# Performance work log

Measured on AMD Instinct MI355X. Metric: run time of the kernel, lower is better.

## Reference

```python
import jax, jax.numpy as jnp
import numpy as np

H = 4
C = 140
N0, E0 = 20000, 320000
N1, E1 = 5000, 80000
N2, E2 = 20000 // 16, 20000
N2, E2 = 1250, 20000
NSAME = 10  # conv02,11,12,21,22,14,15,16,04,05 (all 140->140)


def _seg_mean(v, idx, n):
    s = jax.ops.segment_sum(v, idx, num_segments=n)
    cnt = jax.ops.segment_sum(jnp.ones((idx.shape[0],), v.dtype), idx, num_segments=n)
    return s / jnp.maximum(cnt, 1.0)[:, None]


def _feast_conv(x, ei, W, u, c, b, n):
    # PyG FeaStConv, mean aggregation, no self loops.
    src, dst = ei[0], ei[1]
    xj = x[src]               # (E, Cin) neighbor (source) features
    xi = x[dst]               # (E, Cin) center (target) features
    q = jax.nn.softmax((xj - xi) @ u + c, axis=-1)            # (E, H)
    m = (xj @ W).reshape(xj.shape[0], H, -1)                  # (E, H, Cout)
    msg = jnp.einsum('eh,ehc->ec', q, m)                      # (E, Cout)
    return _seg_mean(msg, dst, n) + b


def _ln(h, g, be):
    mu = h.mean(-1, keepdims=True)
    v = ((h - mu) ** 2).mean(-1, keepdims=True)
    return (h - mu) * jax.lax.rsqrt(v + 1e-5) * g + be


def _block(x, ei, n, W, u, c, b, g=None, be=None, sW=None, sb=None, relu=True):
    h = _feast_conv(x, ei, W, u, c, b, n)
    if g is not None:
        h = _ln(h, g, be)
    skip = x if sW is None else x @ sW + sb
    h = h + skip
    if relu:
        h = jax.nn.relu(h)
    return h


def setup_inputs() -> dict:
    key = jax.random.key(0)
    ks = iter(jax.random.split(key, 80))

    def nrm(shape, s=0.05):
        return jax.random.normal(next(ks), shape, jnp.float32) * s

    inp = {}
    inp['x'] = jax.random.normal(next(ks), (N0, 4), jnp.float32)
    inp['e0'] = jax.random.randint(next(ks), (2, E0), 0, N0)
    inp['e1'] = jax.random.randint(next(ks), (2, E1), 0, N1)
    inp['e2'] = jax.random.randint(next(ks), (2, E2), 0, N2)
    inp['cl1'] = jax.random.randint(next(ks), (N0,), 0, N1)
    inp['cl2'] = jax.random.randint(next(ks), (N1,), 0, N2)
    inp['n0'], inp['n1'], inp['n2'] = N0, N1, N2
    # conv01: 4 -> 140 (linear skip)
    inp['W01'] = nrm((4, H * C)); inp['u01'] = nrm((4, H)); inp['c01'] = nrm((H,))
    inp['b01'] = nrm((C,)); inp['sW01'] = nrm((4, C)); inp['sb01'] = nrm((C,))
    inp['g01'] = jnp.ones((C,)); inp['be01'] = jnp.zeros((C,))
    # 10 stacked 140->140 blocks (identity skip)
    inp['Ws'] = nrm((NSAME, C, H * C)); inp['us'] = nrm((NSAME, C, H))
    inp['cs'] = nrm((NSAME, H)); inp['bs'] = nrm((NSAME, C))
    inp['gs'] = jnp.ones((NSAME, C)); inp['bes'] = jnp.zeros((NSAME, C))
    # 2 concat blocks: 280 -> 140 (conv13, conv03), linear skip
    inp['Wc'] = nrm((2, 2 * C, H * C)); inp['uc'] = nrm((2, 2 * C, H))
    inp['cc'] = nrm((2, H)); inp['bc'] = nrm((2, C))
    inp['sWc'] = nrm((2, 2 * C, C)); inp['sbc'] = nrm((2, C))
    inp['gc'] = jnp.ones((2, C)); inp['bec'] = jnp.zeros((2, C))
    # conv06: 140 -> 1, no LN, no relu, linear skip
    inp['Wo'] = nrm((C, H * 1)); inp['uo'] = nrm((C, H)); inp['co'] = nrm((H,))
    inp['bo'] = nrm((1,)); inp['sWo'] = nrm((C, 1)); inp['sbo'] = nrm((1,))
    return inp


def reference(x, W01, u01, c01, b01, sW01, sb01, g01, be01,
              Ws, us, cs, bs, gs, bes,
              Wc, uc, cc, bc, sWc, sbc, gc, bec,
              Wo, uo, co, bo, sWo, sbo,
              e0, e1, e2, cl1, cl2, n0, n1, n2):
    def same(h, i, ei, n):
        return _block(h, ei, n, Ws[i], us[i], cs[i], bs[i], gs[i], bes[i])

    def catblk(h, i, ei, n):
        return _block(h, ei, n, Wc[i], uc[i], cc[i], bc[i], gc[i], bec[i], sWc[i], sbc[i])

    h = _block(x, e0, n0, W01, u01, c01, b01, g01, be01, sW01, sb01)  # conv01
    h = same(h, 0, e0, n0)                                            # conv02
    copy0 = h
    h1 = _seg_mean(h, cl1, n1)                                        # pool1
    h1 = same(h1, 1, e1, n1)                                          # conv11
    h1 = same(h1, 2, e1, n1)                                          # conv12
    copy1 = h1
    h2 = _seg_mean(h1, cl2, n2)                                       # pool2
    h2 = same(h2, 3, e2, n2)                                          # conv21
    h2 = same(h2, 4, e2, n2)                                          # conv22
    h1 = h2[cl2]                                                      # unpool2
    h1 = jnp.concatenate((h1, copy1), axis=1)
    h1 = catblk(h1, 0, e1, n1)                                        # conv13
    h1 = same(h1, 5, e1, n1)                                          # conv14
    h1 = same(h1, 6, e1, n1)                                          # conv15
    h1 = same(h1, 7, e1, n1)                                          # conv16
    h = h1[cl1]                                                       # unpool1
    h = jnp.concatenate((h, copy0), axis=1)
    h = catblk(h, 1, e0, n0)                                          # conv03
    h = same(h, 8, e0, n0)                                            # conv04
    h = same(h, 9, e0, n0)                                            # conv05
    h = _block(h, e0, n0, Wo, uo, co, bo, None, None, sWo, sbo, relu=False)  # conv06
    return h.reshape(-1, 1)
```

## Files before the change

### kernel.cpp

```cpp
#include <hip/hip_runtime.h>
#include <math.h>

#define HH 4
#define CC 140
#define HALF 160

typedef __attribute__((ext_vector_type(8))) short short8;
typedef __attribute__((ext_vector_type(8))) _Float16 half8;
typedef __attribute__((ext_vector_type(4))) float f32x4;
typedef __attribute__((ext_vector_type(2))) _Float16 h2;
typedef unsigned short u16;

__device__ inline u16 f2h(float x) {
  union { _Float16 h; u16 u; } v; v.h = (_Float16)x; return v.u;
}
__device__ inline float h2f(u16 u) {
  union { _Float16 h; u16 u; } v; v.u = u; return (float)v.h;
}
__device__ inline h2 u2h2(unsigned u) {
  union { unsigned u; h2 h; } v; v.u = u; return v.h;
}
__device__ inline float dot2(h2 a, h2 b, float c) {
#if __has_builtin(__builtin_amdgcn_fdot2)
  return __builtin_amdgcn_fdot2(a, b, c, false);
#else
  return c + (float)a[0] * (float)b[0] + (float)a[1] * (float)b[1];
#endif
}

__global__ __launch_bounds__(256) void k_zero_i32(int* __restrict__ p, int n) {
  int i = blockIdx.x * 256 + threadIdx.x;
  if (i < n) p[i] = 0;
}
__global__ __launch_bounds__(256) void k_hist_all(
    const int* __restrict__ e0, int nE0, const int* __restrict__ e1, int nE1,
    const int* __restrict__ e2, int nE2, const int* __restrict__ cl1, int n0,
    const int* __restrict__ cl2, int n1,
    int* __restrict__ c0, int* __restrict__ c1, int* __restrict__ c2,
    int* __restrict__ c3, int* __restrict__ c4) {
  int j = blockIdx.x * 256 + threadIdx.x;
  if (j < nE0) { atomicAdd(&c0[e0[nE0 + j]], 1); return; }
  j -= nE0;
  if (j < nE1) { atomicAdd(&c1[e1[nE1 + j]], 1); return; }
  j -= nE1;
  if (j < nE2) { atomicAdd(&c2[e2[nE2 + j]], 1); return; }
  j -= nE2;
  if (j < n0) { atomicAdd(&c3[cl1[j]], 1); return; }
  j -= n0;
  if (j < n1) { atomicAdd(&c4[cl2[j]], 1); }
}
__global__ __launch_bounds__(1024) void k_exscan5(
    int* __restrict__ c0, int n0, int* __restrict__ r0,
    int* __restrict__ c1, int n1, int* __restrict__ r1,
    int* __restrict__ c2, int n2, int* __restrict__ r2,
    int* __restrict__ c3, int n3, int* __restrict__ r3,
    int* __restrict__ c4, int n4, int* __restrict__ r4) {
  int* in; int n; int* out;
  switch (blockIdx.x) {
    case 0: in = c0; n = n0; out = r0; break;
    case 1: in = c1; n = n1; out = r1; break;
    case 2: in = c2; n = n2; out = r2; break;
    case 3: in = c3; n = n3; out = r3; break;
    default: in = c4; n = n4; out = r4; break;
  }
  __shared__ int buf[1024];
  __shared__ int carry_s;
  if (threadIdx.x == 0) carry_s = 0;
  __syncthreads();
  for (int base = 0; base < n; base += 1024) {
    int i = base + (int)threadIdx.x;
    int v = (i < n) ? in[i] : 0;
    buf[threadIdx.x] = v;
    __syncthreads();
    int x = v;
    for (int off = 1; off < 1024; off <<= 1) {
      int t = (threadIdx.x >= (unsigned)off) ? buf[threadIdx.x - off] : 0;
      __syncthreads();
      x += t;
      buf[threadIdx.x] = x;
      __syncthreads();
    }
    int carry = carry_s;
    if (i < n) {
      int pref = carry + x - v;
      out[i] = pref;
      in[i] = pref;
    }
    __syncthreads();
    if (threadIdx.x == 1023) carry_s = carry + buf[1023];
    __syncthreads();
  }
  if (threadIdx.x == 0) out[n] = carry_s;
}
__global__ __launch_bounds__(256) void k_scatter_all(
    const int* __restrict__ e0, int nE0, const int* __restrict__ e1, int nE1,
    const int* __restrict__ e2, int nE2, const int* __restrict__ cl1, int n0,
    const int* __restrict__ cl2, int n1,
    int* __restrict__ c0, int* __restrict__ c1, int* __restrict__ c2,
    int* __restrict__ c3, int* __restrict__ c4,
    int* __restrict__ s0, int* __restrict__ s1, int* __restrict__ s2,
    int* __restrict__ s3, int* __restrict__ s4) {
  int j = blockIdx.x * 256 + threadIdx.x;
  if (j < nE0) { int p = atomicAdd(&c0[e0[nE0 + j]], 1); s0[p] = e0[j]; return; }
  j -= nE0;
  if (j < nE1) { int p = atomicAdd(&c1[e1[nE1 + j]], 1); s1[p] = e1[j]; return; }
  j -= nE1;
  if (j < nE2) { int p = atomicAdd(&c2[e2[nE2 + j]], 1); s2[p] = e2[j]; return; }
  j -= nE2;
  if (j < n0) { int p = atomicAdd(&c3[cl1[j]], 1); s3[p] = j; return; }
  j -= n0;
  if (j < n1) { int p = atomicAdd(&c4[cl2[j]], 1); s4[p] = j; }
}

__device__ inline void pack_one(int idx, const float* __restrict__ W,
                                const float* __restrict__ u, const float* __restrict__ sW,
                                u16* __restrict__ out, int C, int K1, int K2, int Kpad) {
  int col = idx / Kpad, kp = idx - col * Kpad;
  int ksrc = -1;
  if (kp < K1) ksrc = kp;
  else if (kp >= HALF && kp - HALF < K2) ksrc = K1 + (kp - HALF);
  float v = 0.f;
  if (ksrc >= 0) {
    if (col < 4 * C) {
      int c = col >> 2, h = col & 3;
      v = W[(size_t)ksrc * 4 * C + h * C + c];
    } else if (col < 4 * C + 4) {
      v = u[(size_t)ksrc * 4 + (col - 4 * C)];
    } else if (sW && col < 5 * C + 4) {
      v = sW[(size_t)ksrc * C + (col - 4 * C - 4)];
    }
  }
  out[idx] = f2h(v);
}
#define P01 (704 * 32)
#define PCAT (704 * 320)
#define PO (64 * 160)
#define PS (576 * 160)
__global__ __launch_bounds__(256) void k_pack_all(
    const float* __restrict__ W01, const float* __restrict__ u01, const float* __restrict__ sW01,
    const float* __restrict__ Wc, const float* __restrict__ uc, const float* __restrict__ sWc,
    const float* __restrict__ Wo, const float* __restrict__ uo, const float* __restrict__ sWo,
    const float* __restrict__ Ws, const float* __restrict__ us,
    const float* __restrict__ x,
    u16* __restrict__ Bp01, u16* __restrict__ Bpc0, u16* __restrict__ Bpc1,
    u16* __restrict__ Bpo, u16* __restrict__ Bps_all, u16* __restrict__ xb, int N0) {
  int j = blockIdx.x * 256 + threadIdx.x;
  if (j < P01) { pack_one(j, W01, u01, sW01, Bp01, CC, 4, 0, 32); return; }
  j -= P01;
  if (j < PCAT) { pack_one(j, Wc, uc, sWc, Bpc0, CC, CC, CC, 320); return; }
  j -= PCAT;
  if (j < PCAT) {
    pack_one(j, Wc + (size_t)2 * CC * HH * CC, uc + (size_t)2 * CC * HH,
             sWc + (size_t)2 * CC * CC, Bpc1, CC, CC, CC, 320);
    return;
  }
  j -= PCAT;
  if (j < PO) { pack_one(j, Wo, uo, sWo, Bpo, 1, CC, 0, 160); return; }
  j -= PO;
  if (j < 10 * PS) {
    int layer = j / PS, r = j - layer * PS;
    pack_one(r, Ws + (size_t)layer * CC * 4 * CC, us + (size_t)layer * CC * 4, nullptr,
             Bps_all + (size_t)layer * PS, CC, CC, 0, 160);
    return;
  }
  j -= 10 * PS;
  if (j < N0 * 32) {
    int i = j >> 5, c = j & 31;
    xb[j] = f2h(c < 4 ? x[(size_t)i * 4 + c] : 0.f);
  }
}

__global__ __launch_bounds__(256) void k_gemm_mfma(
    const u16* __restrict__ A1, const u16* __restrict__ A2,
    const int* __restrict__ amap, const u16* __restrict__ Bp,
    u16* __restrict__ Gy, float* __restrict__ Gl, float* __restrict__ Gs,
    int yEnd, int Cs, int N, int Kpad, int lda1) {
  __shared__ __align__(16) u16 As[128 * 32];
  __shared__ __align__(16) u16 Bs[64 * 32];
  const int tid = threadIdx.x;
  const int row0 = blockIdx.y * 128, col0 = blockIdx.x * 64;
  const int w = tid >> 6, lane = tid & 63;
  const int wm = w >> 1, wn = w & 1;
  const int arow = lane & 15, chunk = lane >> 4;
  const int swz = chunk ^ (arow & 3);
  f32x4 acc[4][2];
#pragma unroll
  for (int i = 0; i < 4; ++i)
#pragma unroll
    for (int j = 0; j < 2; ++j) acc[i][j] = (f32x4){0.f, 0.f, 0.f, 0.f};
  const int sar = tid >> 1;
  const int sak = (tid & 1) * 16;
  const int sbc = tid >> 2;
  const int sbk = (tid & 3) * 8;
  for (int k0 = 0; k0 < Kpad; k0 += 32) {
    {
      int gr = row0 + sar;
      short8 v0 = {0, 0, 0, 0, 0, 0, 0, 0}, v1 = v0;
      if (gr < N) {
        int kp0 = k0 + sak;
        const u16* b_;
        int rr, kk, ld;
        if (A2 && kp0 >= HALF) {
          b_ = A2; rr = gr; kk = kp0 - HALF; ld = HALF;
        } else {
          b_ = A1; rr = amap ? amap[gr] : gr; kk = kp0; ld = lda1;
        }
        const u16* p = b_ + (size_t)rr * ld + kk;
        v0 = *(const short8*)(p);
        v1 = *(const short8*)(p + 8);
      }
      int c0 = sak >> 3, sw = sar & 3;
      *(short8*)(As + sar * 32 + ((c0 ^ sw) << 3)) = v0;
      *(short8*)(As + sar * 32 + (((c0 + 1) ^ sw) << 3)) = v1;
    }
    {
      int gc = col0 + sbc;
      short8 v = *(const short8*)(Bp + (size_t)gc * Kpad + k0 + sbk);
      int c = sbk >> 3, sw = sbc & 3;
      *(short8*)(Bs + sbc * 32 + ((c ^ sw) << 3)) = v;
    }
    __syncthreads();
    half8 bf[2], af[4];
#pragma unroll
    for (int ni = 0; ni < 2; ++ni) {
      int col = wn * 32 + ni * 16 + arow;
      bf[ni] = *(const half8*)(Bs + col * 32 + (swz << 3));
    }
#pragma unroll
    for (int mi = 0; mi < 4; ++mi) {
      int r = wm * 64 + mi * 16 + arow;
      af[mi] = *(const half8*)(As + r * 32 + (swz << 3));
    }
#pragma unroll
    for (int mi = 0; mi < 4; ++mi)
#pragma unroll
      for (int ni = 0; ni < 2; ++ni)
        acc[mi][ni] = __builtin_amdgcn_mfma_f32_16x16x32_f16(af[mi], bf[ni], acc[mi][ni], 0, 0, 0);
    __syncthreads();
  }
  const int crow = (lane >> 4) * 4, ccol = lane & 15;
#pragma unroll
  for (int mi = 0; mi < 4; ++mi) {
    int gr0 = row0 + wm * 64 + mi * 16 + crow;
#pragma unroll
    for (int ni = 0; ni < 2; ++ni) {
      int gc = col0 + wn * 32 + ni * 16 + ccol;
#pragma unroll
      for (int j = 0; j < 4; ++j) {
        int gr = gr0 + j;
        if (gr >= N) continue;
        float v = acc[mi][ni][j];
        if (gc < yEnd) Gy[(size_t)gr * yEnd + gc] = f2h(v);
        else if (gc < yEnd + 4) Gl[(size_t)gr * 4 + (gc - yEnd)] = v;
        else if (gc < yEnd + 4 + Cs) Gs[(size_t)gr * Cs + (gc - yEnd - 4)] = v;
      }
    }
  }
}

__global__ __launch_bounds__(256) void k_agg(
    const u16* __restrict__ Gy, const float* __restrict__ Gl,
    const float* __restrict__ cv, const float* __restrict__ bias,
    const float* __restrict__ g, const float* __restrict__ be,
    const u16* __restrict__ skipA,
    const float* __restrict__ Gs, const float* __restrict__ sb,
    const int* __restrict__ rp, const int* __restrict__ sl,
    u16* __restrict__ outA, int n, int relu) {
  int wid = blockIdx.x * 4 + ((int)threadIdx.x >> 6);
  int lane = threadIdx.x & 63;
  if (wid >= n) return;
  float4 la = *(const float4*)(Gl + (size_t)wid * 4);
  float d0 = cv[0] - la.x, d1 = cv[1] - la.y;
  float d2 = cv[2] - la.z, d3 = cv[3] - la.w;
  int eb = rp[wid], ee = rp[wid + 1];
  const int c0 = lane, c1 = lane + 64, c2 = lane + 128;
  const bool h2v = c2 < CC;
  float acc0 = 0.f, acc1 = 0.f, acc2 = 0.f;
  for (int base = eb; base < ee; base += 64) {
    int m = min(ee - base, 64);
    int sreg = 0;
    int q01 = 0, q23 = 0;
    if (lane < m) {
      sreg = sl[base + lane];
      float4 lg = *(const float4*)(Gl + (size_t)sreg * 4);
      float t0 = lg.x + d0, t1 = lg.y + d1, t2 = lg.z + d2, t3 = lg.w + d3;
      float mx = fmaxf(fmaxf(t0, t1), fmaxf(t2, t3));
      float q0 = __expf(t0 - mx), q1 = __expf(t1 - mx);
      float q2 = __expf(t2 - mx), q3 = __expf(t3 - mx);
      float qi = 1.f / (q0 + q1 + q2 + q3);
      q01 = (int)((unsigned)f2h(q0 * qi) | ((unsigned)f2h(q1 * qi) << 16));
      q23 = (int)((unsigned)f2h(q2 * qi) | ((unsigned)f2h(q3 * qi) << 16));
    }
#pragma unroll 2
    for (int j = 0; j < m; ++j) {
      int s = __shfl(sreg, j);
      h2 p01 = u2h2((unsigned)__shfl(q01, j));
      h2 p23 = u2h2((unsigned)__shfl(q23, j));
      const u16* gy = Gy + (size_t)s * 560;
      uint2 y0 = *(const uint2*)(gy + (c0 << 2));
      acc0 = dot2(u2h2(y0.x), p01, acc0);
      acc0 = dot2(u2h2(y0.y), p23, acc0);
      uint2 y1 = *(const uint2*)(gy + (c1 << 2));
      acc1 = dot2(u2h2(y1.x), p01, acc1);
      acc1 = dot2(u2h2(y1.y), p23, acc1);
      if (h2v) {
        uint2 y2 = *(const uint2*)(gy + (c2 << 2));
        acc2 = dot2(u2h2(y2.x), p01, acc2);
        acc2 = dot2(u2h2(y2.y), p23, acc2);
      }
    }
  }
  int cnt = ee - eb;
  float inv = 1.f / (float)(cnt > 1 ? cnt : 1);
  float v0 = acc0 * inv + bias[c0];
  float v1 = acc1 * inv + bias[c1];
  float v2 = h2v ? acc2 * inv + bias[c2] : 0.f;
  if (g) {
    float s1 = v0 + v1 + v2;
    float s2 = v0 * v0 + v1 * v1 + v2 * v2;
#pragma unroll
    for (int off = 32; off > 0; off >>= 1) {
      s1 += __shfl_xor(s1, off);
      s2 += __shfl_xor(s2, off);
    }
    float mu = s1 * (1.0f / CC);
    float var = s2 * (1.0f / CC) - mu * mu;
    float r = rsqrtf(var + 1e-5f);
    v0 = (v0 - mu) * r * g[c0] + be[c0];
    v1 = (v1 - mu) * r * g[c1] + be[c1];
    if (h2v) v2 = (v2 - mu) * r * g[c2] + be[c2];
  }
  if (skipA) {
    const u16* sk = skipA + (size_t)wid * HALF;
    v0 += h2f(sk[c0]);
    v1 += h2f(sk[c1]);
    if (h2v) v2 += h2f(sk[c2]);
  } else {
    const float* gsr = Gs + (size_t)wid * CC;
    v0 += gsr[c0] + sb[c0];
    v1 += gsr[c1] + sb[c1];
    if (h2v) v2 += gsr[c2] + sb[c2];
  }
  if (relu) {
    v0 = fmaxf(v0, 0.f); v1 = fmaxf(v1, 0.f); v2 = fmaxf(v2, 0.f);
  }
  u16* oa = outA + (size_t)wid * HALF;
  oa[c0] = f2h(v0);
  oa[c1] = f2h(v1);
  if (h2v) oa[c2] = f2h(v2);
  else if (c2 < HALF) oa[c2] = 0;
}

__global__ __launch_bounds__(256) void k_out(
    const u16* __restrict__ Gy, const float* __restrict__ Gl,
    const float* __restrict__ cv, const float* __restrict__ bo,
    const float* __restrict__ Gs, const float* __restrict__ sbo,
    const int* __restrict__ rp, const int* __restrict__ sl,
    float* __restrict__ out, int n) {
  int wid = blockIdx.x * 4 + ((int)threadIdx.x >> 6);
  int lane = threadIdx.x & 63;
  if (wid >= n) return;
  float4 la = *(const float4*)(Gl + (size_t)wid * 4);
  float d0 = cv[0] - la.x, d1 = cv[1] - la.y;
  float d2 = cv[2] - la.z, d3 = cv[3] - la.w;
  int eb = rp[wid], ee = rp[wid + 1];
  float part = 0.f;
  for (int e = eb + lane; e < ee; e += 64) {
    int s = sl[e];
    float4 lg = *(const float4*)(Gl + (size_t)s * 4);
    float t0 = lg.x + d0, t1 = lg.y + d1, t2 = lg.z + d2, t3 = lg.w + d3;
    float m = fmaxf(fmaxf(t0, t1), fmaxf(t2, t3));
    float q0 = __expf(t0 - m), q1 = __expf(t1 - m), q2 = __expf(t2 - m), q3 = __expf(t3 - m);
    float qi = 1.f / (q0 + q1 + q2 + q3);
    uint2 y = *(const uint2*)(Gy + (size_t)s * 4);
    h2 y01 = u2h2(y.x), y23 = u2h2(y.y);
    part += (q0 * (float)y01[0] + q1 * (float)y01[1] +
             q2 * (float)y23[0] + q3 * (float)y23[1]) * qi;
  }
#pragma unroll
  for (int off = 32; off > 0; off >>= 1) part += __shfl_xor(part, off);
  if (lane == 0) {
    int cnt = ee - eb;
    out[wid] = part / (float)(cnt > 1 ? cnt : 1) + bo[0] + Gs[wid] + sbo[0];
  }
}

__global__ __launch_bounds__(256) void k_pool(const u16* __restrict__ inA,
                                              const int* __restrict__ rp,
                                              const int* __restrict__ sl,
                                              u16* __restrict__ outA, int nseg) {
  int wid = blockIdx.x * 4 + ((int)threadIdx.x >> 6);
  int lane = threadIdx.x & 63;
  if (wid >= nseg) return;
  int a = rp[wid], b = rp[wid + 1];
  const int c0 = lane, c1 = lane + 64, c2 = lane + 128;
  const bool h2v = c2 < CC;
  float acc0 = 0.f, acc1 = 0.f, acc2 = 0.f;
  for (int s = a; s < b; ++s) {
    size_t off = (size_t)sl[s] * HALF;
    acc0 += h2f(inA[off + c0]);
    acc1 += h2f(inA[off + c1]);
    if (h2v) acc2 += h2f(inA[off + c2]);
  }
  int cnt = b - a;
  float inv = 1.f / (float)(cnt > 1 ? cnt : 1);
  u16* oa = outA + (size_t)wid * HALF;
  oa[c0] = f2h(acc0 * inv);
  oa[c1] = f2h(acc1 * inv);
  if (h2v) oa[c2] = f2h(acc2 * inv);
  else if (c2 < HALF) oa[c2] = 0;
}

extern "C" void kernel_launch(void* const* d_in, const int* in_sizes, int n_in,
                              void* d_out, int out_size, void* d_ws, size_t ws_size,
                              hipStream_t stream) {
  (void)n_in; (void)out_size;
  const float* x    = (const float*)d_in[0];
  const int*   e0   = (const int*)d_in[1];
  const int*   e1   = (const int*)d_in[2];
  const int*   e2   = (const int*)d_in[3];
  const int*   cl1  = (const int*)d_in[4];
  const int*   cl2  = (const int*)d_in[5];
  const float* W01  = (const float*)d_in[9];
  const float* u01  = (const float*)d_in[10];
  const float* c01  = (const float*)d_in[11];
  const float* b01  = (const float*)d_in[12];
  const float* sW01 = (const float*)d_in[13];
  const float* sb01 = (const float*)d_in[14];
  const float* g01  = (const float*)d_in[15];
  const float* be01 = (const float*)d_in[16];
  const float* Ws   = (const float*)d_in[17];
  const float* us   = (const float*)d_in[18];
  const float* cs   = (const float*)d_in[19];
  const float* bs   = (const float*)d_in[20];
  const float* gs   = (const float*)d_in[21];
  const float* bes  = (const float*)d_in[22];
  const float* Wc   = (const float*)d_in[23];
  const float* uc   = (const float*)d_in[24];
  const float* cc   = (const float*)d_in[25];
  const float* bc   = (const float*)d_in[26];
  const float* sWc  = (const float*)d_in[27];
  const float* sbc  = (const float*)d_in[28];
  const float* gc   = (const float*)d_in[29];
  const float* bec  = (const float*)d_in[30];
  const float* Wo   = (const float*)d_in[31];
  const float* uo   = (const float*)d_in[32];
  const float* co   = (const float*)d_in[33];
  const float* bo   = (const float*)d_in[34];
  const float* sWo  = (const float*)d_in[35];
  const float* sbo  = (const float*)d_in[36];

  const int N0 = in_sizes[0] / 4;
  const int nE0 = in_sizes[1] / 2;
  const int nE1 = in_sizes[2] / 2;
  const int nE2 = in_sizes[3] / 2;
  const int N1 = 5000, N2 = 1250;

  float* fp = (float*)d_ws;
  auto alloc_f = [&](size_t n) { n = (n + 15) & ~(size_t)15; float* p = fp; fp += n; return p; };
  auto alloc_h = [&](size_t n) { return (u16*)alloc_f((n + 1) / 2); };
  u16*   Gy = alloc_h((size_t)N0 * 560);
  float* Gl = alloc_f((size_t)N0 * 4);
  float* Gs = alloc_f((size_t)N0 * CC);
  u16* a0A = alloc_h((size_t)N0 * HALF);
  u16* a0B = alloc_h((size_t)N0 * HALF);
  u16* a1A = alloc_h((size_t)N1 * HALF);
  u16* a1B = alloc_h((size_t)N1 * HALF);
  u16* a2A = alloc_h((size_t)N2 * HALF);
  u16* a2B = alloc_h((size_t)N2 * HALF);
  u16* xb  = alloc_h((size_t)N0 * 32);
  u16* Bp01 = alloc_h(P01);
  u16* Bpc0 = alloc_h(PCAT);
  u16* Bpc1 = alloc_h(PCAT);
  u16* Bpo  = alloc_h(PO);
  u16* Bps_all = alloc_h((size_t)10 * PS);
  u16* Bps[10];
  for (int i = 0; i < 10; ++i) Bps[i] = Bps_all + (size_t)i * PS;
  int* ipb = (int*)fp;
  auto alloc_i = [&](size_t n) { int* p = ipb; ipb += n; return p; };
  int* rp0  = alloc_i(N0 + 1);
  int* sl0  = alloc_i(nE0);
  int* rp1  = alloc_i(N1 + 1);
  int* sl1  = alloc_i(nE1);
  int* rp2  = alloc_i(N2 + 1);
  int* sl2  = alloc_i(nE2);
  int* rpc1 = alloc_i(N1 + 1);
  int* slc1 = alloc_i(N0);
  int* rpc2 = alloc_i(N2 + 1);
  int* slc2 = alloc_i(N1);
  int* cur0 = alloc_i(N0);
  int* cur1 = alloc_i(N1);
  int* cur2 = alloc_i(N2);
  int* cur3 = alloc_i(N1);
  int* cur4 = alloc_i(N2);
  const int curTot = N0 + N1 + N2 + N1 + N2;
  if ((size_t)((char*)ipb - (char*)d_ws) > ws_size) return;

  auto cdiv = [](int a, int b) { return (a + b - 1) / b; };

  k_zero_i32<<<cdiv(curTot, 256), 256, 0, stream>>>(cur0, curTot);
  {
    int tot = nE0 + nE1 + nE2 + N0 + N1;
    k_hist_all<<<cdiv(tot, 256), 256, 0, stream>>>(e0, nE0, e1, nE1, e2, nE2, cl1, N0, cl2, N1,
                                                   cur0, cur1, cur2, cur3, cur4);
    k_exscan5<<<5, 1024, 0, stream>>>(cur0, N0, rp0, cur1, N1, rp1, cur2, N2, rp2,
                                      cur3, N1, rpc1, cur4, N2, rpc2);
    k_scatter_all<<<cdiv(tot, 256), 256, 0, stream>>>(e0, nE0, e1, nE1, e2, nE2, cl1, N0, cl2, N1,
                                                      cur0, cur1, cur2, cur3, cur4,
                                                      sl0, sl1, sl2, slc1, slc2);
  }
  {
    int tot = P01 + 2 * PCAT + PO + 10 * PS + N0 * 32;
    k_pack_all<<<cdiv(tot, 256), 256, 0, stream>>>(W01, u01, sW01, Wc, uc, sWc, Wo, uo, sWo,
                                                   Ws, us, x, Bp01, Bpc0, Bpc1, Bpo,
                                                   Bps_all, xb, N0);
  }

  auto do_conv = [&](const u16* A1, const u16* A2, const int* amap, int Kpad, int lda1,
                     const u16* Bp, int Mld, bool hasSkip, int n, const int* rp, const int* sl,
                     const float* cp, const float* bp, const float* gp, const float* bep,
                     const u16* skipA, const float* sbp, u16* outA) {
    dim3 grid(Mld / 64, cdiv(n, 128));
    k_gemm_mfma<<<grid, 256, 0, stream>>>(A1, A2, amap, Bp, Gy, Gl, Gs,
                                          560, hasSkip ? CC : 0, n, Kpad, lda1);
    k_agg<<<cdiv(n, 4), 256, 0, stream>>>(Gy, Gl, cp, bp, gp, bep, skipA, Gs, sbp,
                                          rp, sl, outA, n, 1);
  };

  auto ci  = [&](int i) { return cs + (size_t)i * HH; };
  auto bi  = [&](int i) { return bs + (size_t)i * CC; };
  auto gi  = [&](int i) { return gs + (size_t)i * CC; };
  auto bei = [&](int i) { return bes + (size_t)i * CC; };

  do_conv(xb, nullptr, nullptr, 32, 32, Bp01, 704, true, N0, rp0, sl0,
          c01, b01, g01, be01, nullptr, sb01, a0A);
  do_conv(a0A, nullptr, nullptr, 160, HALF, Bps[0], 576, false, N0, rp0, sl0,
          ci(0), bi(0), gi(0), bei(0), a0A, nullptr, a0B);
  k_pool<<<cdiv(N1, 4), 256, 0, stream>>>(a0B, rpc1, slc1, a1A, N1);
  do_conv(a1A, nullptr, nullptr, 160, HALF, Bps[1], 576, false, N1, rp1, sl1,
          ci(1), bi(1), gi(1), bei(1), a1A, nullptr, a1B);
  do_conv(a1B, nullptr, nullptr, 160, HALF, Bps[2], 576, false, N1, rp1, sl1,
          ci(2), bi(2), gi(2), bei(2), a1B, nullptr, a1A);
  k_pool<<<cdiv(N2, 4), 256, 0, stream>>>(a1A, rpc2, slc2, a2A, N2);
  do_conv(a2A, nullptr, nullptr, 160, HALF, Bps[3], 576, false, N2, rp2, sl2,
          ci(3), bi(3), gi(3), bei(3), a2A, nullptr, a2B);
  do_conv(a2B, nullptr, nullptr, 160, HALF, Bps[4], 576, false, N2, rp2, sl2,
          ci(4), bi(4), gi(4), bei(4), a2B, nullptr, a2A);
  do_conv(a2A, a1A, cl2, 320, HALF, Bpc0, 704, true, N1, rp1, sl1,
          cc, bc, gc, bec, nullptr, sbc, a1B);
  do_conv(a1B, nullptr, nullptr, 160, HALF, Bps[5], 576, false, N1, rp1, sl1,
          ci(5), bi(5), gi(5), bei(5), a1B, nullptr, a1A);
  do_conv(a1A, nullptr, nullptr, 160, HALF, Bps[6], 576, false, N1, rp1, sl1,
          ci(6), bi(6), gi(6), bei(6), a1A, nullptr, a1B);
  do_conv(a1B, nullptr, nullptr, 160, HALF, Bps[7], 576, false, N1, rp1, sl1,
          ci(7), bi(7), gi(7), bei(7), a1B, nullptr, a1A);
  do_conv(a1A, a0B, cl1, 320, HALF, Bpc1, 704, true, N0, rp0, sl0,
          cc + HH, bc + CC, gc + CC, bec + CC, nullptr, sbc + CC, a0A);
  do_conv(a0A, nullptr, nullptr, 160, HALF, Bps[8], 576, false, N0, rp0, sl0,
          ci(8), bi(8), gi(8), bei(8), a0A, nullptr, a0B);
  do_conv(a0B, nullptr, nullptr, 160, HALF, Bps[9], 576, false, N0, rp0, sl0,
          ci(9), bi(9), gi(9), bei(9), a0B, nullptr, a0A);
  {
    dim3 grid(1, cdiv(N0, 128));
    k_gemm_mfma<<<grid, 256, 0, stream>>>(a0A, nullptr, nullptr, Bpo, Gy, Gl, Gs,
                                          4, 1, N0, 160, HALF);
    k_out<<<cdiv(N0, 4), 256, 0, stream>>>(Gy, Gl, co, bo, Gs, sbo, rp0, sl0, (float*)d_out, N0);
  }
}
```

Measured before the change: 713.2 us.

## Aggregate raw neighbor features per head before the weight GEMM

Each FeaStConv is reordered so the softmax-weighted neighbor features are summed per head first (k_aggz writes a per-node 4x144 tensor z), and the W projection then runs as a per-node GEMM (k_gemm2) that also fuses mean scaling, bias, LayerNorm, skip and ReLU. The goal is to stop computing and storing the per-node 560-wide projected features that the old edge gather read in full, cutting gather traffic and GEMM work on large graphs. In exchange it adds a kernel per conv, a 576-wide fp16 z buffer and scalar fp32 FMA accumulation of 12 products per edge per lane. The concat convs need two aggregation passes through a cluster map.

```diff
diff --git a/kernel.cpp b/kernel.cpp
--- a/kernel.cpp
+++ b/kernel.cpp
@@ -19,13 +19,6 @@
 }
 __device__ inline h2 u2h2(unsigned u) {
   union { unsigned u; h2 h; } v; v.u = u; return v.h;
-}
-__device__ inline float dot2(h2 a, h2 b, float c) {
-#if __has_builtin(__builtin_amdgcn_fdot2)
-  return __builtin_amdgcn_fdot2(a, b, c, false);
-#else
-  return c + (float)a[0] * (float)b[0] + (float)a[1] * (float)b[1];
-#endif
 }
 
 __global__ __launch_bounds__(256) void k_zero_i32(int* __restrict__ p, int n) {
@@ -112,61 +105,107 @@
   if (j < n1) { int p = atomicAdd(&c4[cl2[j]], 1); s4[p] = j; }
 }
 
-__device__ inline void pack_one(int idx, const float* __restrict__ W,
-                                const float* __restrict__ u, const float* __restrict__ sW,
-                                u16* __restrict__ out, int C, int K1, int K2, int Kpad) {
-  int col = idx / Kpad, kp = idx - col * Kpad;
-  int ksrc = -1;
-  if (kp < K1) ksrc = kp;
-  else if (kp >= HALF && kp - HALF < K2) ksrc = K1 + (kp - HALF);
-  float v = 0.f;
-  if (ksrc >= 0) {
-    if (col < 4 * C) {
-      int c = col >> 2, h = col & 3;
-      v = W[(size_t)ksrc * 4 * C + h * C + c];
-    } else if (col < 4 * C + 4) {
-      v = u[(size_t)ksrc * 4 + (col - 4 * C)];
-    } else if (sW && col < 5 * C + 4) {
-      v = sW[(size_t)ksrc * C + (col - 4 * C - 4)];
-    }
-  }
-  out[idx] = f2h(v);
-}
-#define P01 (704 * 32)
-#define PCAT (704 * 320)
-#define PO (64 * 160)
-#define PS (576 * 160)
-__global__ __launch_bounds__(256) void k_pack_all(
-    const float* __restrict__ W01, const float* __restrict__ u01, const float* __restrict__ sW01,
-    const float* __restrict__ Wc, const float* __restrict__ uc, const float* __restrict__ sWc,
-    const float* __restrict__ Wo, const float* __restrict__ uo, const float* __restrict__ sWo,
-    const float* __restrict__ Ws, const float* __restrict__ us,
-    const float* __restrict__ x,
-    u16* __restrict__ Bp01, u16* __restrict__ Bpc0, u16* __restrict__ Bpc1,
-    u16* __restrict__ Bpo, u16* __restrict__ Bps_all, u16* __restrict__ xb, int N0) {
+#define S01 (192 * 32)
+#define SS  (64 * 160)
+#define SC  (192 * 320)
+#define SO  (64 * 160)
+__global__ __launch_bounds__(256) void k_pack1(
+    const float* __restrict__ u01, const float* __restrict__ sW01,
+    const float* __restrict__ us, const float* __restrict__ uc,
+    const float* __restrict__ sWc,
+    const float* __restrict__ Wo, const float* __restrict__ uo,
+    const float* __restrict__ sWo, const float* __restrict__ x,
+    u16* __restrict__ B01, u16* __restrict__ Bs10, u16* __restrict__ Bc2,
+    u16* __restrict__ Bpo, u16* __restrict__ xb, int N0) {
   int j = blockIdx.x * 256 + threadIdx.x;
-  if (j < P01) { pack_one(j, W01, u01, sW01, Bp01, CC, 4, 0, 32); return; }
-  j -= P01;
-  if (j < PCAT) { pack_one(j, Wc, uc, sWc, Bpc0, CC, CC, CC, 320); return; }
-  j -= PCAT;
-  if (j < PCAT) {
-    pack_one(j, Wc + (size_t)2 * CC * HH * CC, uc + (size_t)2 * CC * HH,
-             sWc + (size_t)2 * CC * CC, Bpc1, CC, CC, CC, 320);
+  if (j < S01) {
+    int col = j / 32, kp = j % 32;
+    float v = 0.f;
+    if (kp < 4) {
+      if (col < 4) v = u01[kp * 4 + col];
+      else if (col < 144) v = sW01[kp * 140 + col - 4];
+    }
+    B01[j] = f2h(v);
     return;
   }
-  j -= PCAT;
-  if (j < PO) { pack_one(j, Wo, uo, sWo, Bpo, 1, CC, 0, 160); return; }
-  j -= PO;
-  if (j < 10 * PS) {
-    int layer = j / PS, r = j - layer * PS;
-    pack_one(r, Ws + (size_t)layer * CC * 4 * CC, us + (size_t)layer * CC * 4, nullptr,
-             Bps_all + (size_t)layer * PS, CC, CC, 0, 160);
+  j -= S01;
+  if (j < 10 * SS) {
+    int r = j % SS, layer = j / SS;
+    int col = r / 160, kp = r % 160;
+    float v = 0.f;
+    if (kp < 140 && col < 4) v = us[(size_t)layer * 560 + kp * 4 + col];
+    Bs10[j] = f2h(v);
     return;
   }
-  j -= 10 * PS;
+  j -= 10 * SS;
+  if (j < 2 * SC) {
+    int layer = j / SC, r = j % SC;
+    int col = r / 320, kp = r % 320;
+    int ksrc = (kp < 140) ? kp : ((kp >= 160 && kp < 300) ? 140 + (kp - 160) : -1);
+    float v = 0.f;
+    if (ksrc >= 0) {
+      if (col < 4) v = uc[(size_t)layer * 1120 + ksrc * 4 + col];
+      else if (col < 144) v = sWc[(size_t)layer * 39200 + ksrc * 140 + col - 4];
+    }
+    Bc2[j] = f2h(v);
+    return;
+  }
+  j -= 2 * SC;
+  if (j < SO) {
+    int col = j / 160, kp = j % 160;
+    float v = 0.f;
+    if (kp < 140) {
+      if (col < 4) v = Wo[kp * 4 + (col & 3)];
+      else if (col < 8) v = uo[kp * 4 + (col - 4)];
+      else if (col == 8) v = sWo[kp];
+    }
+    Bpo[j] = f2h(v);
+    return;
+  }
+  j -= SO;
   if (j < N0 * 32) {
     int i = j >> 5, c = j & 31;
     xb[j] = f2h(c < 4 ? x[(size_t)i * 4 + c] : 0.f);
+  }
+}
+
+#define T01 (160 * 32)
+#define TS  (160 * 576)
+#define TC  (160 * 1152)
+__global__ __launch_bounds__(256) void k_pack2(
+    const float* __restrict__ W01, const float* __restrict__ Ws,
+    const float* __restrict__ Wc,
+    u16* __restrict__ Q01, u16* __restrict__ Qs10, u16* __restrict__ Qc2) {
+  int j = blockIdx.x * 256 + threadIdx.x;
+  if (j < T01) {
+    int col = j / 32, kp = j % 32;
+    int h = kp >> 3, kin = kp & 7;
+    float v = (col < 140 && kin < 4) ? W01[kin * 560 + h * 140 + col] : 0.f;
+    Q01[j] = f2h(v);
+    return;
+  }
+  j -= T01;
+  if (j < 10 * TS) {
+    int layer = j / TS, r = j % TS;
+    int col = r / 576, kp = r % 576;
+    int h = kp / 144, kin = kp % 144;
+    float v = (col < 140 && kin < 140)
+                  ? Ws[(size_t)layer * 78400 + (size_t)kin * 560 + h * 140 + col]
+                  : 0.f;
+    Qs10[j] = f2h(v);
+    return;
+  }
+  j -= 10 * TS;
+  if (j < 2 * TC) {
+    int layer = j / TC, r = j % TC;
+    int col = r / 1152, kp = r % 1152;
+    int half = kp / 576, kph = kp % 576;
+    int h = kph / 144, kin = kph % 144;
+    int src = half ? 140 + kin : kin;
+    float v = (col < 140 && kin < 140)
+                  ? Wc[(size_t)layer * 156800 + (size_t)src * 560 + h * 140 + col]
+                  : 0.f;
+    Qc2[j] = f2h(v);
   }
 }
 
@@ -258,14 +297,13 @@
   }
 }
 
-__global__ __launch_bounds__(256) void k_agg(
-    const u16* __restrict__ Gy, const float* __restrict__ Gl,
-    const float* __restrict__ cv, const float* __restrict__ bias,
-    const float* __restrict__ g, const float* __restrict__ be,
-    const u16* __restrict__ skipA,
-    const float* __restrict__ Gs, const float* __restrict__ sb,
+__global__ __launch_bounds__(256) void k_aggz(
+    const u16* __restrict__ X, int ldx, int Cin,
+    const int* __restrict__ amap,
+    const float* __restrict__ Gl, const float* __restrict__ cv,
     const int* __restrict__ rp, const int* __restrict__ sl,
-    u16* __restrict__ outA, int n, int relu) {
+    u16* __restrict__ z, int ldz, int hs,
+    float* __restrict__ invd, int n) {
   int wid = blockIdx.x * 4 + ((int)threadIdx.x >> 6);
   int lane = threadIdx.x & 63;
   if (wid >= n) return;
@@ -274,15 +312,18 @@
   float d2 = cv[2] - la.z, d3 = cv[3] - la.w;
   int eb = rp[wid], ee = rp[wid + 1];
   const int c0 = lane, c1 = lane + 64, c2 = lane + 128;
-  const bool h2v = c2 < CC;
-  float acc0 = 0.f, acc1 = 0.f, acc2 = 0.f;
+  float acc[4][3];
+#pragma unroll
+  for (int h = 0; h < 4; ++h)
+#pragma unroll
+    for (int s = 0; s < 3; ++s) acc[h][s] = 0.f;
   for (int base = eb; base < ee; base += 64) {
     int m = min(ee - base, 64);
-    int sreg = 0;
-    int q01 = 0, q23 = 0;
+    int rreg = 0, q01 = 0, q23 = 0;
     if (lane < m) {
-      sreg = sl[base + lane];
-      float4 lg = *(const float4*)(Gl + (size_t)sreg * 4);
+      int s = sl[base + lane];
+      rreg = amap ? amap[s] : s;
+      float4 lg = *(const float4*)(Gl + (size_t)s * 4);
       float t0 = lg.x + d0, t1 = lg.y + d1, t2 = lg.z + d2, t3 = lg.w + d3;
       float mx = fmaxf(fmaxf(t0, t1), fmaxf(t2, t3));
       float q0 = __expf(t0 - mx), q1 = __expf(t1 - mx);
@@ -293,62 +334,152 @@
     }
 #pragma unroll 2
     for (int j = 0; j < m; ++j) {
-      int s = __shfl(sreg, j);
-      h2 p01 = u2h2((unsigned)__shfl(q01, j));
-      h2 p23 = u2h2((unsigned)__shfl(q23, j));
-      const u16* gy = Gy + (size_t)s * 560;
-      uint2 y0 = *(const uint2*)(gy + (c0 << 2));
-      acc0 = dot2(u2h2(y0.x), p01, acc0);
-      acc0 = dot2(u2h2(y0.y), p23, acc0);
-      uint2 y1 = *(const uint2*)(gy + (c1 << 2));
-      acc1 = dot2(u2h2(y1.x), p01, acc1);
-      acc1 = dot2(u2h2(y1.y), p23, acc1);
-      if (h2v) {
-        uint2 y2 = *(const uint2*)(gy + (c2 << 2));
-        acc2 = dot2(u2h2(y2.x), p01, acc2);
-        acc2 = dot2(u2h2(y2.y), p23, acc2);
+      int r = __shfl(rreg, j);
+      h2 h01 = u2h2((unsigned)__shfl(q01, j));
+      h2 h23 = u2h2((unsigned)__shfl(q23, j));
+      float q0 = (float)h01[0], q1 = (float)h01[1];
+      float q2 = (float)h23[0], q3 = (float)h23[1];
+      const u16* xr = X + (size_t)r * ldx;
+      float x0 = (c0 < Cin) ? h2f(xr[c0]) : 0.f;
+      float x1 = (c1 < Cin) ? h2f(xr[c1]) : 0.f;
+      float x2 = (c2 < Cin) ? h2f(xr[c2]) : 0.f;
+      acc[0][0] += q0 * x0; acc[0][1] += q0 * x1; acc[0][2] += q0 * x2;
+      acc[1][0] += q1 * x0; acc[1][1] += q1 * x1; acc[1][2] += q1 * x2;
+      acc[2][0] += q2 * x0; acc[2][1] += q2 * x1; acc[2][2] += q2 * x2;
+      acc[3][0] += q3 * x0; acc[3][1] += q3 * x1; acc[3][2] += q3 * x2;
+    }
+  }
+  u16* zr = z + (size_t)wid * ldz;
+#pragma unroll
+  for (int h = 0; h < 4; ++h) {
+    if (c0 < Cin) zr[h * hs + c0] = f2h(acc[h][0]);
+    else if (c0 < hs) zr[h * hs + c0] = 0;
+    if (c1 < Cin) zr[h * hs + c1] = f2h(acc[h][1]);
+    else if (c1 < hs) zr[h * hs + c1] = 0;
+    if (c2 < Cin) zr[h * hs + c2] = f2h(acc[h][2]);
+    else if (c2 < hs) zr[h * hs + c2] = 0;
+  }
+  if (lane == 0) {
+    int cnt = ee - eb;
+    invd[wid] = 1.f / (float)(cnt > 1 ? cnt : 1);
+  }
+}
+
+__global__ __launch_bounds__(256) void k_gemm2(
+    const u16* __restrict__ A1, const u16* __restrict__ A2, int lda,
+    const u16* __restrict__ Bp, int Kpad,
+    const float* __restrict__ invd, const float* __restrict__ bias,
+    const float* __restrict__ g, const float* __restrict__ be,
+    const u16* __restrict__ skipA, const float* __restrict__ Gs,
+    const float* __restrict__ sb,
+    u16* __restrict__ H, int n) {
+  __shared__ __align__(16) u16 As[128 * 32];
+  __shared__ __align__(16) u16 Bs[160 * 32];
+  const int tid = threadIdx.x;
+  const int row0 = blockIdx.x * 128;
+  const int w = tid >> 6, lane = tid & 63;
+  const int arow = lane & 15, chunk = lane >> 4;
+  const int swz = chunk ^ (arow & 3);
+  f32x4 acc[2][10];
+#pragma unroll
+  for (int mi = 0; mi < 2; ++mi)
+#pragma unroll
+    for (int ni = 0; ni < 10; ++ni) acc[mi][ni] = (f32x4){0.f, 0.f, 0.f, 0.f};
+  const int sar = tid >> 1;
+  const int sak = (tid & 1) * 16;
+  for (int k0 = 0; k0 < Kpad; k0 += 32) {
+    {
+      int gr = row0 + sar;
+      short8 v0 = {0, 0, 0, 0, 0, 0, 0, 0}, v1 = v0;
+      if (gr < n) {
+        int kp0 = k0 + sak;
+        const u16* b_ = A1;
+        int kk = kp0;
+        if (A2 && kp0 >= 576) { b_ = A2; kk = kp0 - 576; }
+        const u16* p = b_ + (size_t)gr * lda + kk;
+        v0 = *(const short8*)(p);
+        v1 = *(const short8*)(p + 8);
       }
-    }
-  }
-  int cnt = ee - eb;
-  float inv = 1.f / (float)(cnt > 1 ? cnt : 1);
-  float v0 = acc0 * inv + bias[c0];
-  float v1 = acc1 * inv + bias[c1];
-  float v2 = h2v ? acc2 * inv + bias[c2] : 0.f;
-  if (g) {
-    float s1 = v0 + v1 + v2;
-    float s2 = v0 * v0 + v1 * v1 + v2 * v2;
-#pragma unroll
-    for (int off = 32; off > 0; off >>= 1) {
-      s1 += __shfl_xor(s1, off);
-      s2 += __shfl_xor(s2, off);
-    }
-    float mu = s1 * (1.0f / CC);
-    float var = s2 * (1.0f / CC) - mu * mu;
-    float r = rsqrtf(var + 1e-5f);
-    v0 = (v0 - mu) * r * g[c0] + be[c0];
-    v1 = (v1 - mu) * r * g[c1] + be[c1];
-    if (h2v) v2 = (v2 - mu) * r * g[c2] + be[c2];
-  }
-  if (skipA) {
-    const u16* sk = skipA + (size_t)wid * HALF;
-    v0 += h2f(sk[c0]);
-    v1 += h2f(sk[c1]);
-    if (h2v) v2 += h2f(sk[c2]);
-  } else {
-    const float* gsr = Gs + (size_t)wid * CC;
-    v0 += gsr[c0] + sb[c0];
-    v1 += gsr[c1] + sb[c1];
-    if (h2v) v2 += gsr[c2] + sb[c2];
-  }
-  if (relu) {
-    v0 = fmaxf(v0, 0.f); v1 = fmaxf(v1, 0.f); v2 = fmaxf(v2, 0.f);
-  }
-  u16* oa = outA + (size_t)wid * HALF;
-  oa[c0] = f2h(v0);
-  oa[c1] = f2h(v1);
-  if (h2v) oa[c2] = f2h(v2);
-  else if (c2 < HALF) oa[c2] = 0;
+      int c0 = sak >> 3, sw = sar & 3;
+      *(short8*)(As + sar * 32 + ((c0 ^ sw) << 3)) = v0;
+      *(short8*)(As + sar * 32 + (((c0 + 1) ^ sw) << 3)) = v1;
+    }
+#pragma unroll
+    for (int it = 0; it < 3; ++it) {
+      int i = tid + it * 256;
+      if (i < 640) {
+        int col = i >> 2, kf = (i & 3) * 8;
+        short8 v = *(const short8*)(Bp + (size_t)col * Kpad + k0 + kf);
+        *(short8*)(Bs + col * 32 + (((kf >> 3) ^ (col & 3)) << 3)) = v;
+      }
+    }
+    __syncthreads();
+    half8 af0, af1;
+    {
+      int r = w * 32 + arow;
+      af0 = *(const half8*)(As + r * 32 + (swz << 3));
+      af1 = *(const half8*)(As + (r + 16) * 32 + (swz << 3));
+    }
+#pragma unroll
+    for (int ni = 0; ni < 10; ++ni) {
+      int col = ni * 16 + arow;
+      half8 bf = *(const half8*)(Bs + col * 32 + (swz << 3));
+      acc[0][ni] = __builtin_amdgcn_mfma_f32_16x16x32_f16(af0, bf, acc[0][ni], 0, 0, 0);
+      acc[1][ni] = __builtin_amdgcn_mfma_f32_16x16x32_f16(af1, bf, acc[1][ni], 0, 0, 0);
+    }
+    __syncthreads();
+  }
+  const int colL = arow, grp = lane >> 4;
+  float bcol[10], gcol[10], becol[10], sbcol[10];
+#pragma unroll
+  for (int ni = 0; ni < 10; ++ni) {
+    int c = ni * 16 + colL;
+    bool ok = c < CC;
+    bcol[ni] = ok ? bias[c] : 0.f;
+    gcol[ni] = ok ? g[c] : 0.f;
+    becol[ni] = ok ? be[c] : 0.f;
+    sbcol[ni] = (sb != nullptr && ok) ? sb[c] : 0.f;
+  }
+#pragma unroll
+  for (int mi = 0; mi < 2; ++mi) {
+#pragma unroll
+    for (int j = 0; j < 4; ++j) {
+      int gr = row0 + w * 32 + mi * 16 + grp * 4 + j;
+      bool rowok = gr < n;
+      float iv = rowok ? invd[gr] : 0.f;
+      float vals[10];
+      float s1 = 0.f, s2 = 0.f;
+#pragma unroll
+      for (int ni = 0; ni < 10; ++ni) {
+        float v = acc[mi][ni][j] * iv + bcol[ni];
+        vals[ni] = v;
+        s1 += v;
+        s2 += v * v;
+      }
+      s1 += __shfl_xor(s1, 1); s2 += __shfl_xor(s2, 1);
+      s1 += __shfl_xor(s1, 2); s2 += __shfl_xor(s2, 2);
+      s1 += __shfl_xor(s1, 4); s2 += __shfl_xor(s2, 4);
+      s1 += __shfl_xor(s1, 8); s2 += __shfl_xor(s2, 8);
+      float mu = s1 * (1.0f / CC);
+      float var = s2 * (1.0f / CC) - mu * mu;
+      float rstd = rsqrtf(var + 1e-5f);
+      if (rowok) {
+#pragma unroll
+        for (int ni = 0; ni < 10; ++ni) {
+          int c = ni * 16 + colL;
+          if (c < CC) {
+            float v = (vals[ni] - mu) * rstd * gcol[ni] + becol[ni];
+            float sk = skipA ? h2f(skipA[(size_t)gr * HALF + c])
+                             : (Gs[(size_t)gr * CC + c] + sbcol[ni]);
+            v = fmaxf(v + sk, 0.f);
+            H[(size_t)gr * HALF + c] = f2h(v);
+          } else {
+            H[(size_t)gr * HALF + c] = 0;
+          }
+        }
+      }
+    }
+  }
 }
 
 __global__ __launch_bounds__(256) void k_out(
@@ -459,9 +590,12 @@
   float* fp = (float*)d_ws;
   auto alloc_f = [&](size_t n) { n = (n + 15) & ~(size_t)15; float* p = fp; fp += n; return p; };
   auto alloc_h = [&](size_t n) { return (u16*)alloc_f((n + 1) / 2); };
-  u16*   Gy = alloc_h((size_t)N0 * 560);
+  u16*   Gy = alloc_h((size_t)N0 * 8);
   float* Gl = alloc_f((size_t)N0 * 4);
   float* Gs = alloc_f((size_t)N0 * CC);
+  float* invd = alloc_f((size_t)N0);
+  u16* zA = alloc_h((size_t)N0 * 576);
+  u16* zB = alloc_h((size_t)N0 * 576);
   u16* a0A = alloc_h((size_t)N0 * HALF);
   u16* a0B = alloc_h((size_t)N0 * HALF);
   u16* a1A = alloc_h((size_t)N1 * HALF);
@@ -469,13 +603,13 @@
   u16* a2A = alloc_h((size_t)N2 * HALF);
   u16* a2B = alloc_h((size_t)N2 * HALF);
   u16* xb  = alloc_h((size_t)N0 * 32);
-  u16* Bp01 = alloc_h(P01);
-  u16* Bpc0 = alloc_h(PCAT);
-  u16* Bpc1 = alloc_h(PCAT);
-  u16* Bpo  = alloc_h(PO);
-  u16* Bps_all = alloc_h((size_t)10 * PS);
-  u16* Bps[10];
-  for (int i = 0; i < 10; ++i) Bps[i] = Bps_all + (size_t)i * PS;
+  u16* B01  = alloc_h(S01);
+  u16* Bs10 = alloc_h((size_t)10 * SS);
+  u16* Bc2  = alloc_h((size_t)2 * SC);
+  u16* Bpo  = alloc_h(SO);
+  u16* Q01  = alloc_h(T01);
+  u16* Qs10 = alloc_h((size_t)10 * TS);
+  u16* Qc2  = alloc_h((size_t)2 * TC);
   int* ipb = (int*)fp;
   auto alloc_i = [&](size_t n) { int* p = ipb; ipb += n; return p; };
   int* rp0  = alloc_i(N0 + 1);
@@ -510,60 +644,78 @@
                                                       sl0, sl1, sl2, slc1, slc2);
   }
   {
-    int tot = P01 + 2 * PCAT + PO + 10 * PS + N0 * 32;
-    k_pack_all<<<cdiv(tot, 256), 256, 0, stream>>>(W01, u01, sW01, Wc, uc, sWc, Wo, uo, sWo,
-                                                   Ws, us, x, Bp01, Bpc0, Bpc1, Bpo,
-                                                   Bps_all, xb, N0);
-  }
-
-  auto do_conv = [&](const u16* A1, const u16* A2, const int* amap, int Kpad, int lda1,
-                     const u16* Bp, int Mld, bool hasSkip, int n, const int* rp, const int* sl,
-                     const float* cp, const float* bp, const float* gp, const float* bep,
-                     const u16* skipA, const float* sbp, u16* outA) {
-    dim3 grid(Mld / 64, cdiv(n, 128));
-    k_gemm_mfma<<<grid, 256, 0, stream>>>(A1, A2, amap, Bp, Gy, Gl, Gs,
-                                          560, hasSkip ? CC : 0, n, Kpad, lda1);
-    k_agg<<<cdiv(n, 4), 256, 0, stream>>>(Gy, Gl, cp, bp, gp, bep, skipA, Gs, sbp,
-                                          rp, sl, outA, n, 1);
-  };
+    int tot1 = S01 + 10 * SS + 2 * SC + SO + N0 * 32;
+    k_pack1<<<cdiv(tot1, 256), 256, 0, stream>>>(u01, sW01, us, uc, sWc, Wo, uo, sWo, x,
+                                                 B01, Bs10, Bc2, Bpo, xb, N0);
+    int tot2 = T01 + 10 * TS + 2 * TC;
+    k_pack2<<<cdiv(tot2, 256), 256, 0, stream>>>(W01, Ws, Wc, Q01, Qs10, Qc2);
+  }
 
   auto ci  = [&](int i) { return cs + (size_t)i * HH; };
   auto bi  = [&](int i) { return bs + (size_t)i * CC; };
   auto gi  = [&](int i) { return gs + (size_t)i * CC; };
   auto bei = [&](int i) { return bes + (size_t)i * CC; };
 
-  do_conv(xb, nullptr, nullptr, 32, 32, Bp01, 704, true, N0, rp0, sl0,
-          c01, b01, g01, be01, nullptr, sb01, a0A);
-  do_conv(a0A, nullptr, nullptr, 160, HALF, Bps[0], 576, false, N0, rp0, sl0,
-          ci(0), bi(0), gi(0), bei(0), a0A, nullptr, a0B);
+  auto conv_plain = [&](const u16* aIn, const u16* Bp1, const u16* Bq, int n,
+                        const int* rp, const int* sl, const float* cv,
+                        const float* bp, const float* gp, const float* bep, u16* aOut) {
+    dim3 g1(1, cdiv(n, 128));
+    k_gemm_mfma<<<g1, 256, 0, stream>>>(aIn, nullptr, nullptr, Bp1, Gy, Gl, Gs,
+                                        0, 0, n, 160, HALF);
+    k_aggz<<<cdiv(n, 4), 256, 0, stream>>>(aIn, HALF, 140, nullptr, Gl, cv, rp, sl,
+                                           zA, 576, 144, invd, n);
+    k_gemm2<<<cdiv(n, 128), 256, 0, stream>>>(zA, nullptr, 576, Bq, 576, invd,
+                                              bp, gp, bep, aIn, nullptr, nullptr, aOut, n);
+  };
+
+  {
+    dim3 g1(3, cdiv(N0, 128));
+    k_gemm_mfma<<<g1, 256, 0, stream>>>(xb, nullptr, nullptr, B01, Gy, Gl, Gs,
+                                        0, 140, N0, 32, 32);
+    k_aggz<<<cdiv(N0, 4), 256, 0, stream>>>(xb, 32, 4, nullptr, Gl, c01, rp0, sl0,
+                                            zA, 32, 8, invd, N0);
+    k_gemm2<<<cdiv(N0, 128), 256, 0, stream>>>(zA, nullptr, 32, Q01, 32, invd,
+                                               b01, g01, be01, nullptr, Gs, sb01, a0A, N0);
+  }
+  conv_plain(a0A, Bs10 + 0 * SS, Qs10 + (size_t)0 * TS, N0, rp0, sl0, ci(0), bi(0), gi(0), bei(0), a0B);
   k_pool<<<cdiv(N1, 4), 256, 0, stream>>>(a0B, rpc1, slc1, a1A, N1);
-  do_conv(a1A, nullptr, nullptr, 160, HALF, Bps[1], 576, false, N1, rp1, sl1,
-          ci(1), bi(1), gi(1), bei(1), a1A, nullptr, a1B);
-  do_conv(a1B, nullptr, nullptr, 160, HALF, Bps[2], 576, false, N1, rp1, sl1,
-          ci(2), bi(2), gi(2), bei(2), a1B, nullptr, a1A);
+  conv_plain(a1A, Bs10 + 1 * SS, Qs10 + (size_t)1 * TS, N1, rp1, sl1, ci(1), bi(1), gi(1), bei(1), a1B);
+  conv_plain(a1B, Bs10 + 2 * SS, Qs10 + (size_t)2 * TS, N1, rp1, sl1, ci(2), bi(2), gi(2), bei(2), a1A);
   k_pool<<<cdiv(N2, 4), 256, 0, stream>>>(a1A, rpc2, slc2, a2A, N2);
-  do_conv(a2A, nullptr, nullptr, 160, HALF, Bps[3], 576, false, N2, rp2, sl2,
-          ci(3), bi(3), gi(3), bei(3), a2A, nullptr, a2B);
-  do_conv(a2B, nullptr, nullptr, 160, HALF, Bps[4], 576, false, N2, rp2, sl2,
-          ci(4), bi(4), gi(4), bei(4), a2B, nullptr, a2A);
-  do_conv(a2A, a1A, cl2, 320, HALF, Bpc0, 704, true, N1, rp1, sl1,
-          cc, bc, gc, bec, nullptr, sbc, a1B);
-  do_conv(a1B, nullptr, nullptr, 160, HALF, Bps[5], 576, false, N1, rp1, sl1,
-          ci(5), bi(5), gi(5), bei(5), a1B, nullptr, a1A);
-  do_conv(a1A, nullptr, nullptr, 160, HALF, Bps[6], 576, false, N1, rp1, sl1,
-          ci(6), bi(6), gi(6), bei(6), a1A, nullptr, a1B);
-  do_conv(a1B, nullptr, nullptr, 160, HALF, Bps[7], 576, false, N1, rp1, sl1,
-          ci(7), bi(7), gi(7), bei(7), a1B, nullptr, a1A);
-  do_conv(a1A, a0B, cl1, 320, HALF, Bpc1, 704, true, N0, rp0, sl0,
-          cc + HH, bc + CC, gc + CC, bec + CC, nullptr, sbc + CC, a0A);
-  do_conv(a0A, nullptr, nullptr, 160, HALF, Bps[8], 576, false, N0, rp0, sl0,
-          ci(8), bi(8), gi(8), bei(8), a0A, nullptr, a0B);
-  do_conv(a0B, nullptr, nullptr, 160, HALF, Bps[9], 576, false, N0, rp0, sl0,
-          ci(9), bi(9), gi(9), bei(9), a0B, nullptr, a0A);
+  conv_plain(a2A, Bs10 + 3 * SS, Qs10 + (size_t)3 * TS, N2, rp2, sl2, ci(3), bi(3), gi(3), bei(3), a2B);
+  conv_plain(a2B, Bs10 + 4 * SS, Qs10 + (size_t)4 * TS, N2, rp2, sl2, ci(4), bi(4), gi(4), bei(4), a2A);
   {
-    dim3 grid(1, cdiv(N0, 128));
-    k_gemm_mfma<<<grid, 256, 0, stream>>>(a0A, nullptr, nullptr, Bpo, Gy, Gl, Gs,
-                                          4, 1, N0, 160, HALF);
+    dim3 g1(3, cdiv(N1, 128));
+    k_gemm_mfma<<<g1, 256, 0, stream>>>(a2A, a1A, cl2, Bc2 + 0 * SC, Gy, Gl, Gs,
+                                        0, 140, N1, 320, HALF);
+    k_aggz<<<cdiv(N1, 4), 256, 0, stream>>>(a2A, HALF, 140, cl2, Gl, cc, rp1, sl1,
+                                            zA, 576, 144, invd, N1);
+    k_aggz<<<cdiv(N1, 4), 256, 0, stream>>>(a1A, HALF, 140, nullptr, Gl, cc, rp1, sl1,
+                                            zB, 576, 144, invd, N1);
+    k_gemm2<<<cdiv(N1, 128), 256, 0, stream>>>(zA, zB, 576, Qc2 + (size_t)0 * TC, 1152, invd,
+                                               bc, gc, bec, nullptr, Gs, sbc, a1B, N1);
+  }
+  conv_plain(a1B, Bs10 + 5 * SS, Qs10 + (size_t)5 * TS, N1, rp1, sl1, ci(5), bi(5), gi(5), bei(5), a1A);
+  conv_plain(a1A, Bs10 + 6 * SS, Qs10 + (size_t)6 * TS, N1, rp1, sl1, ci(6), bi(6), gi(6), bei(6), a1B);
+  conv_plain(a1B, Bs10 + 7 * SS, Qs10 + (size_t)7 * TS, N1, rp1, sl1, ci(7), bi(7), gi(7), bei(7), a1A);
+  {
+    dim3 g1(3, cdiv(N0, 128));
+    k_gemm_mfma<<<g1, 256, 0, stream>>>(a1A, a0B, cl1, Bc2 + 1 * SC, Gy, Gl, Gs,
+                                        0, 140, N0, 320, HALF);
+    k_aggz<<<cdiv(N0, 4), 256, 0, stream>>>(a1A, HALF, 140, cl1, Gl, cc + HH, rp0, sl0,
+                                            zA, 576, 144, invd, N0);
+    k_aggz<<<cdiv(N0, 4), 256, 0, stream>>>(a0B, HALF, 140, nullptr, Gl, cc + HH, rp0, sl0,
+                                            zB, 576, 144, invd, N0);
+    k_gemm2<<<cdiv(N0, 128), 256, 0, stream>>>(zA, zB, 576, Qc2 + (size_t)1 * TC, 1152, invd,
+                                               bc + CC, gc + CC, bec + CC, nullptr, Gs, sbc + CC,
+                                               a0A, N0);
+  }
+  conv_plain(a0A, Bs10 + 8 * SS, Qs10 + (size_t)8 * TS, N0, rp0, sl0, ci(8), bi(8), gi(8), bei(8), a0B);
+  conv_plain(a0B, Bs10 + 9 * SS, Qs10 + (size_t)9 * TS, N0, rp0, sl0, ci(9), bi(9), gi(9), bei(9), a0A);
+  {
+    dim3 g1(1, cdiv(N0, 128));
+    k_gemm_mfma<<<g1, 256, 0, stream>>>(a0A, nullptr, nullptr, Bpo, Gy, Gl, Gs,
+                                        4, 1, N0, 160, HALF);
     k_out<<<cdiv(N0, 4), 256, 0, stream>>>(Gy, Gl, co, bo, Gs, sbo, rp0, sl0, (float*)d_out, N0);
   }
 }
```

New measurement: 1.379 ms. +93.4%, slower.
